# Optimization experiments

Measured on AMD Instinct MI355X. Metric: run time of the kernel, lower is better.

## Reference

```python
import jax, jax.numpy as jnp
import numpy as np

B, T, C = 2, 1024, 2048
N, K = 8, 32            # channels, latents per channel
N_HEAD, N_KV, D = 16, 4, 128  # head_dim = C // n_head; n_rep = 4
N_REP = N_HEAD // N_KV
N_LAYERS = 32


def setup_inputs() -> dict:
    key = jax.random.key(0)
    ks = jax.random.split(key, 8)
    std = 0.02
    proj_std = 0.02 / np.sqrt(2 * N_LAYERS)
    return {
        "x": jax.random.normal(ks[0], (B, T, C), jnp.float32),
        "channel_states": jax.random.normal(ks[1], (B, N, K, C), jnp.float32),
        "channel_mask": jax.random.randint(ks[2], (B, T), 0, N, jnp.int32),
        "Wq": jax.random.normal(ks[3], (C, N_HEAD * D), jnp.float32) * std,
        "Wk": jax.random.normal(ks[4], (C, N_KV * D), jnp.float32) * std,
        "Wv": jax.random.normal(ks[5], (C, N_KV * D), jnp.float32) * std,
        "Wo": jax.random.normal(ks[6], (N_HEAD * D, C), jnp.float32) * proj_std,
        "gate": jax.random.normal(ks[7], (1,), jnp.float32) * 0.02,
    }


def reference(x, channel_states, channel_mask, Wq, Wk, Wv, Wo, gate):
    # x: (B,T,C); channel_states: (B,N,K,C); channel_mask: (B,T) in [0,N)
    b, t, c = x.shape
    # Q projection, grouped for GQA: (B,T,n_kv,n_rep,D)
    q = (x @ Wq).reshape(b, t, N_KV, N_REP, D)
    # Project channel latents ONCE per channel (linear, identical math to the
    # module's redundant per-token re-projection): (B,N,K,n_kv,D)
    k = jnp.einsum("bnkc,ce->bnke", channel_states, Wk).reshape(b, N, K, N_KV, D)
    v = jnp.einsum("bnkc,ce->bnke", channel_states, Wv).reshape(b, N, K, N_KV, D)
    # Per-token channel gather: (B,T,K,n_kv,D)
    batch_idx = jnp.arange(b)[:, None]
    sel_k = k[batch_idx, channel_mask]
    sel_v = v[batch_idx, channel_mask]
    # Tiny-K attention per token; GQA expressed via grouped einsum (no repeat).
    scale = 1.0 / jnp.sqrt(jnp.asarray(D, x.dtype))
    scores = jnp.einsum("btgrd,btkgd->btgrk", q, sel_k) * scale  # (B,T,g,r,K)
    attn = jax.nn.softmax(scores, axis=-1)
    y = jnp.einsum("btgrk,btkgd->btgrd", attn, sel_v).reshape(b, t, c)
    out = (y @ Wo) * jnp.tanh(gate)
    return out


if __name__ == "__main__":
    inp = setup_inputs()
    print(reference(**inp).shape)
```

## Files before the change

kernel.cpp:

```cpp
#include <hip/hip_runtime.h>
#include <hip/hip_bf16.h>

#define BB 2
#define TT 1024
#define CC 2048
#define NCH 8
#define KLAT 32
#define NKV 4
#define NREP 4
#define DD 128
#define MROWS (BB*TT)
#define CSROWS (BB*NCH*KLAT)
#define NBUCKET 16
#define TTILE 8
#define MAXTILES (MROWS/TTILE + NBUCKET)

typedef unsigned short u16;
typedef __attribute__((ext_vector_type(8))) short bf16x8;
typedef __attribute__((ext_vector_type(4))) float f32x4;
typedef __attribute__((ext_vector_type(8))) u16 u16x8;

__device__ __forceinline__ u16 f2bf(float f) {
    unsigned int u = __builtin_bit_cast(unsigned int, f);
    u = (u + 0x7FFFu + ((u >> 16) & 1u)) >> 16;
    return (u16)u;
}

__device__ __forceinline__ void glds16(const u16* g, u16* l) {
    __builtin_amdgcn_global_load_lds(
        (const __attribute__((address_space(1))) void*)g,
        (__attribute__((address_space(3))) void*)l, 16, 0, 0);
}

#define PB_SORT 0
#define PB_X    1
#define PB_CS   (PB_X + 2048)
#define PB_WQ   (PB_CS + 512)
#define PB_WK   (PB_WQ + 1024)
#define PB_WV   (PB_WK + 256)
#define PB_WO   (PB_WV + 256)
#define PB_END  (PB_WO + 1024)

__device__ __forceinline__ void cvt_body(const float* __restrict__ in, u16* __restrict__ out,
                                         int blk, int tid) {
    int i = (blk * 256 + tid) * 8;
    float4 a = *(const float4*)(in + i);
    float4 b = *(const float4*)(in + i + 4);
    u16x8 o;
    o[0]=f2bf(a.x); o[1]=f2bf(a.y); o[2]=f2bf(a.z); o[3]=f2bf(a.w);
    o[4]=f2bf(b.x); o[5]=f2bf(b.y); o[6]=f2bf(b.z); o[7]=f2bf(b.w);
    *(u16x8*)(out + i) = o;
}

__device__ __forceinline__ void tcvt_body(const float* __restrict__ in, u16* __restrict__ out,
                                          int R, int C, int bx, int by, int tid,
                                          u16 (*tile)[65]) {
    const int c0 = bx * 64, r0 = by * 64;
    const int tx = tid & 15, ty = tid >> 4;
#pragma unroll
    for (int p = 0; p < 4; ++p) {
        int r = p * 16 + ty;
        float4 v = *(const float4*)(in + (size_t)(r0 + r) * C + c0 + tx * 4);
        tile[tx*4+0][r] = f2bf(v.x);
        tile[tx*4+1][r] = f2bf(v.y);
        tile[tx*4+2][r] = f2bf(v.z);
        tile[tx*4+3][r] = f2bf(v.w);
    }
    __syncthreads();
    const int oc = tid >> 2, op = tid & 3;
    u16* dst = out + (size_t)(c0 + oc) * R + r0 + op * 16;
    u16x8 v0, v1;
#pragma unroll
    for (int j = 0; j < 8; ++j) { v0[j] = tile[oc][op*16 + j]; v1[j] = tile[oc][op*16 + 8 + j]; }
    *(u16x8*)dst = v0;
    *(u16x8*)(dst + 8) = v1;
}

__global__ void __launch_bounds__(256)
prep_kernel(const float* __restrict__ x, const float* __restrict__ cs,
            const int* __restrict__ cm,
            const float* __restrict__ Wq, const float* __restrict__ Wk,
            const float* __restrict__ Wv, const float* __restrict__ Wo,
            u16* __restrict__ xb, u16* __restrict__ csb,
            u16* __restrict__ wqt, u16* __restrict__ wkvt, u16* __restrict__ wot,
            int* __restrict__ sorted, int4* __restrict__ tiles, int* __restrict__ ntiles)
{
    __shared__ u16 tile[64][65];
    __shared__ int cnt[NBUCKET], cur[NBUCKET];
    const int bid = blockIdx.x;
    const int tid = threadIdx.x;

    if (bid == PB_SORT) {
        if (tid < NBUCKET) cnt[tid] = 0;
        __syncthreads();
        for (int i = tid; i < MROWS; i += 256) {
            int bkt = ((i >> 10) << 3) | cm[i];
            atomicAdd(&cnt[bkt], 1);
        }
        __syncthreads();
        if (tid == 0) {
            int off = 0, nt = 0;
            for (int b2 = 0; b2 < NBUCKET; ++b2) {
                cur[b2] = off;
                for (int o = 0; o < cnt[b2]; o += TTILE)
                    tiles[nt++] = make_int4(b2, off + o, min(TTILE, cnt[b2] - o), 0);
                off += cnt[b2];
            }
            *ntiles = nt;
        }
        __syncthreads();
        for (int i = tid; i < MROWS; i += 256) {
            int bkt = ((i >> 10) << 3) | cm[i];
            int pos = atomicAdd(&cur[bkt], 1);
            sorted[pos] = i;
        }
    } else if (bid < PB_CS) {
        cvt_body(x, xb, bid - PB_X, tid);
    } else if (bid < PB_WQ) {
        cvt_body(cs, csb, bid - PB_CS, tid);
    } else if (bid < PB_WK) {
        int b2 = bid - PB_WQ;
        tcvt_body(Wq, wqt, CC, CC, b2 & 31, b2 >> 5, tid, tile);
    } else if (bid < PB_WV) {
        int b2 = bid - PB_WK;
        tcvt_body(Wk, wkvt, CC, 512, b2 & 7, b2 >> 3, tid, tile);
    } else if (bid < PB_WO) {
        int b2 = bid - PB_WV;
        tcvt_body(Wv, wkvt + (size_t)512 * CC, CC, 512, b2 & 7, b2 >> 3, tid, tile);
    } else {
        int b2 = bid - PB_WO;
        tcvt_body(Wo, wot, CC, CC, b2 & 31, b2 >> 5, tid, tile);
    }
}

#define GK 2048
__device__ __forceinline__ void gemm_core(const u16* __restrict__ A, const u16* __restrict__ Bt,
                                          u16* lds, f32x4 (*acc)[4])
{
    constexpr int BK = 32, STAGE = 8192;
    const int tid  = threadIdx.x;
    const int wave = tid >> 6;
    const int lane = tid & 63;
    const int wm = (wave & 1) * 64;
    const int wn = (wave >> 1) * 64;
    const int ml = lane & 15;
    const int quad = lane >> 4;

#pragma unroll
    for (int i = 0; i < 4; ++i)
#pragma unroll
        for (int j = 0; j < 4; ++j) acc[i][j] = (f32x4){0.f, 0.f, 0.f, 0.f};

    const u16* aptr = A  + (size_t)(tid >> 2) * GK + (tid & 3) * 8;
    const u16* bptr = Bt + (size_t)(tid >> 2) * GK + (tid & 3) * 8;
    const int aoff = wave * 512;
    const int boff = 128 * BK + wave * 512;

#pragma unroll
    for (int s = 0; s < 3; ++s) {
        u16* base = lds + s * STAGE;
        glds16(aptr + s * BK,                   base + aoff);
        glds16(aptr + (size_t)64 * GK + s * BK, base + aoff + 2048);
        glds16(bptr + s * BK,                   base + boff);
        glds16(bptr + (size_t)64 * GK + s * BK, base + boff + 2048);
    }

    for (int k0 = 0; k0 < GK; k0 += BK) {
        u16* cbase = lds + ((k0 / BK) & 3) * STAGE;
        asm volatile("s_waitcnt vmcnt(8)" ::: "memory");
        asm volatile("s_barrier" ::: "memory");
        {
            const int kn = k0 + 3 * BK;
            u16* nbase = lds + (((k0 / BK) + 3) & 3) * STAGE;
            glds16(aptr + kn,                   nbase + aoff);
            glds16(aptr + (size_t)64 * GK + kn, nbase + aoff + 2048);
            glds16(bptr + kn,                   nbase + boff);
            glds16(bptr + (size_t)64 * GK + kn, nbase + boff + 2048);
        }
        bf16x8 afr[4], bfr[4];
#pragma unroll
        for (int i = 0; i < 4; ++i)
            afr[i] = *(const bf16x8*)&cbase[(wm + i * 16 + ml) * BK + quad * 8];
#pragma unroll
        for (int j = 0; j < 4; ++j)
            bfr[j] = *(const bf16x8*)&cbase[128 * BK + (wn + j * 16 + ml) * BK + quad * 8];
#pragma unroll
        for (int i = 0; i < 4; ++i)
#pragma unroll
            for (int j = 0; j < 4; ++j)
                acc[i][j] = __builtin_amdgcn_mfma_f32_16x16x32_bf16(afr[i], bfr[j], acc[i][j], 0, 0, 0);
    }
    asm volatile("s_waitcnt vmcnt(0)" ::: "memory");
}

__global__ void __launch_bounds__(256)
gemm_qkv_kernel(const u16* __restrict__ xb, const u16* __restrict__ wqt, u16* __restrict__ qb,
                const u16* __restrict__ csb, const u16* __restrict__ wkvt,
                u16* __restrict__ kb, u16* __restrict__ vt)
{
    constexpr int STAGE = 8192;
    __shared__ u16 lds[4 * STAGE];
    const int bid = blockIdx.x;
    const int tid = threadIdx.x;
    const int wave = tid >> 6, lane = tid & 63;
    const int wm = (wave & 1) * 64, wn = (wave >> 1) * 64;
    const int ml = lane & 15, quad = lane >> 4;
    const bool isQ = bid < 256;
    const u16 *A, *Bt;
    int m0, n0;
    if (isQ) { m0 = (bid & 15) * 128; n0 = (bid >> 4) * 128; A = xb + (size_t)m0 * GK; Bt = wqt + (size_t)n0 * GK; }
    else     { int b2 = bid - 256; m0 = (b2 & 3) * 128; n0 = (b2 >> 2) * 128; A = csb + (size_t)m0 * GK; Bt = wkvt + (size_t)n0 * GK; }

    f32x4 acc[4][4];
    gemm_core(A, Bt, lds, acc);

#pragma unroll
    for (int i = 0; i < 4; ++i)
#pragma unroll
        for (int j = 0; j < 4; ++j)
#pragma unroll
            for (int rr = 0; rr < 4; ++rr) {
                int gr = m0 + wm + i * 16 + quad * 4 + rr;
                int gc = n0 + wn + j * 16 + ml;
                float val = acc[i][j][rr];
                if (isQ) {
                    qb[(size_t)gr * 2048 + gc] = f2bf(val);
                } else if (gc < 512) {
                    kb[(size_t)gr * 512 + gc] = f2bf(val);
                } else {
                    int g = (gc - 512) >> 7, d = (gc - 512) & 127;
                    int bn = gr >> 5, lat = gr & 31;
                    vt[(((size_t)bn * 4 + g) << 12) + (d << 5) + lat] = f2bf(val);
                }
            }
}

__global__ void __launch_bounds__(256)
gemm_out_kernel(const u16* __restrict__ yb, const u16* __restrict__ wot,
                float* __restrict__ out, const float* __restrict__ gate)
{
    constexpr int STAGE = 8192;
    __shared__ u16 lds[4 * STAGE];
    const int tid = threadIdx.x;
    const int wave = tid >> 6, lane = tid & 63;
    const int wm = (wave & 1) * 64, wn = (wave >> 1) * 64;
    const int ml = lane & 15, quad = lane >> 4;
    const int m0 = blockIdx.x * 128, n0 = blockIdx.y * 128;

    f32x4 acc[4][4];
    gemm_core(yb + (size_t)m0 * GK, wot + (size_t)n0 * GK, lds, acc);

    const float scl = tanhf(gate[0]);
#pragma unroll
    for (int i = 0; i < 4; ++i)
#pragma unroll
        for (int j = 0; j < 4; ++j)
#pragma unroll
            for (int rr = 0; rr < 4; ++rr) {
                int gr = m0 + wm + i * 16 + quad * 4 + rr;
                int gc = n0 + wn + j * 16 + ml;
                out[(size_t)gr * 2048 + gc] = acc[i][j][rr] * scl;
            }
}

#define KSTR 136
#define VSTR 40
__global__ void __launch_bounds__(64)
attn_mfma_kernel(const u16* __restrict__ qb, const u16* __restrict__ kb,
                 const u16* __restrict__ vt, const int* __restrict__ sorted,
                 const int4* __restrict__ tiles, const int* __restrict__ ntiles,
                 u16* __restrict__ yb)
{
    const int tile = blockIdx.x;
    if (tile >= *ntiles) return;
    const int g = blockIdx.y;
    const int4 td = tiles[tile];
    const int bucket = td.x, start = td.y, cnt = td.z;
    const int lane = threadIdx.x;
    const int ml = lane & 15, quad = lane >> 4;

    __shared__ u16 k_lds[32 * KSTR];
    __shared__ u16 v_lds[128 * VSTR];
    __shared__ u16 p_lds[32 * VSTR];
    __shared__ int tok_s[TTILE];

    if (lane < TTILE) tok_s[lane] = (lane < cnt) ? sorted[start + lane] : -1;

    {
        const u16* ksrc = kb + (size_t)bucket * 32 * 512 + g * 128;
        const u16* vsrc = vt + ((size_t)bucket * 4 + g) * 4096;
#pragma unroll
        for (int rr = 0; rr < 8; ++rr) {
            int f = rr * 64 + lane;
            int krow = f >> 4, kc = (f & 15) * 8;
            *(u16x8*)&k_lds[krow * KSTR + kc] = *(const u16x8*)(ksrc + (size_t)krow * 512 + kc);
            int vd = f >> 2, vc = (f & 3) * 8;
            *(u16x8*)&v_lds[vd * VSTR + vc] = *(const u16x8*)(vsrc + (size_t)f * 8);
        }
    }
    __syncthreads();

    f32x4 sc[2][2];
#pragma unroll
    for (int i = 0; i < 2; ++i)
#pragma unroll
        for (int j = 0; j < 2; ++j) sc[i][j] = (f32x4){0.f, 0.f, 0.f, 0.f};
    const int tokA = tok_s[ml & 7];
    const u16* qrow = qb + (size_t)(tokA >= 0 ? tokA : 0) * 2048 + g * 512 + (ml >> 3) * 128;
#pragma unroll
    for (int s = 0; s < 4; ++s) {
        bf16x8 bfr0 = *(const bf16x8*)&k_lds[ml * KSTR + s * 32 + quad * 8];
        bf16x8 bfr1 = *(const bf16x8*)&k_lds[(16 + ml) * KSTR + s * 32 + quad * 8];
#pragma unroll
        for (int i = 0; i < 2; ++i) {
            bf16x8 afr = *(const bf16x8*)(qrow + i * 256 + s * 32 + quad * 8);
            sc[i][0] = __builtin_amdgcn_mfma_f32_16x16x32_bf16(afr, bfr0, sc[i][0], 0, 0, 0);
            sc[i][1] = __builtin_amdgcn_mfma_f32_16x16x32_bf16(afr, bfr1, sc[i][1], 0, 0, 0);
        }
    }

    const float scale = 0.088388347648318447f;
#pragma unroll
    for (int i = 0; i < 2; ++i)
#pragma unroll
        for (int reg = 0; reg < 4; ++reg) {
            float s0 = sc[i][0][reg] * scale;
            float s1 = sc[i][1][reg] * scale;
            float mx = fmaxf(s0, s1);
            mx = fmaxf(mx, __shfl_xor(mx, 1));
            mx = fmaxf(mx, __shfl_xor(mx, 2));
            mx = fmaxf(mx, __shfl_xor(mx, 4));
            mx = fmaxf(mx, __shfl_xor(mx, 8));
            float e0 = __expf(s0 - mx), e1 = __expf(s1 - mx);
            float sm = e0 + e1;
            sm += __shfl_xor(sm, 1);
            sm += __shfl_xor(sm, 2);
            sm += __shfl_xor(sm, 4);
            sm += __shfl_xor(sm, 8);
            float inv = 1.0f / sm;
            int prow = i * 16 + quad * 4 + reg;
            p_lds[prow * VSTR + ml]      = f2bf(e0 * inv);
            p_lds[prow * VSTR + 16 + ml] = f2bf(e1 * inv);
        }
    __syncthreads();

    bf16x8 pfr[2], vfr[8];
    pfr[0] = *(const bf16x8*)&p_lds[ml * VSTR + quad * 8];
    pfr[1] = *(const bf16x8*)&p_lds[(16 + ml) * VSTR + quad * 8];
#pragma unroll
    for (int j = 0; j < 8; ++j)
        vfr[j] = *(const bf16x8*)&v_lds[(j * 16 + ml) * VSTR + quad * 8];
#pragma unroll
    for (int i = 0; i < 2; ++i)
#pragma unroll
        for (int j = 0; j < 8; ++j) {
            f32x4 o = (f32x4){0.f, 0.f, 0.f, 0.f};
            o = __builtin_amdgcn_mfma_f32_16x16x32_bf16(pfr[i], vfr[j], o, 0, 0, 0);
#pragma unroll
            for (int reg = 0; reg < 4; ++reg) {
                int m = quad * 4 + reg;
                int tok = tok_s[m & 7];
                if (tok >= 0) {
                    int r = i * 2 + (m >> 3);
                    yb[(size_t)tok * 2048 + g * 512 + r * 128 + j * 16 + ml] = f2bf(o[reg]);
                }
            }
        }
}

extern "C" void kernel_launch(void* const* d_in, const int* in_sizes, int n_in,
                              void* d_out, int out_size, void* d_ws, size_t ws_size,
                              hipStream_t stream) {
    const float* x    = (const float*)d_in[0];
    const float* cs   = (const float*)d_in[1];
    const int*   cm   = (const int*)d_in[2];
    const float* Wq   = (const float*)d_in[3];
    const float* Wk   = (const float*)d_in[4];
    const float* Wv   = (const float*)d_in[5];
    const float* Wo   = (const float*)d_in[6];
    const float* gate = (const float*)d_in[7];
    float* out = (float*)d_out;

    char* w = (char*)d_ws;
    u16* xb   = (u16*)w;  w += (size_t)MROWS * CC * 2;
    u16* wqt  = (u16*)w;  w += (size_t)CC * CC * 2;
    u16* wot  = (u16*)w;  w += (size_t)CC * CC * 2;
    u16* qb   = (u16*)w;  w += (size_t)MROWS * CC * 2;
    u16* yb   = (u16*)w;  w += (size_t)MROWS * CC * 2;
    u16* csb  = (u16*)w;  w += (size_t)CSROWS * CC * 2;
    u16* wkvt = (u16*)w;  w += (size_t)1024 * CC * 2;
    u16* kb   = (u16*)w;  w += (size_t)CSROWS * 512 * 2;
    u16* vt   = (u16*)w;  w += (size_t)64 * 128 * 32 * 2;
    int* sorted = (int*)w; w += (size_t)MROWS * 4;
    int4* tiles = (int4*)w; w += (size_t)MAXTILES * 16;
    int* ntiles = (int*)w;  w += 4096;

    prep_kernel<<<PB_END, 256, 0, stream>>>(x, cs, cm, Wq, Wk, Wv, Wo,
                                            xb, csb, wqt, wkvt, wot,
                                            sorted, tiles, ntiles);
    gemm_qkv_kernel<<<288, 256, 0, stream>>>(xb, wqt, qb, csb, wkvt, kb, vt);
    attn_mfma_kernel<<<dim3(MAXTILES, 4), 64, 0, stream>>>(qb, kb, vt, sorted, tiles, ntiles, yb);
    gemm_out_kernel<<<dim3(16, 16), 256, 0, stream>>>(yb, wot, out, gate);
}
```

Measured before the change: 196.3 us.

## Fold split-K KV projection into Q GEMM blocks and swizzle GEMM tile order

The QKV launch goes from 288 blocks to 256. Each block first computes its Q tile, then one eighth of the K dimension for a KV tile, writing fp32 partial sums. A new combine kernel sums the eight partials and writes K and the transposed V in bf16. This is meant to remove the second-wave tail that the 32 full-K KV blocks caused, at the cost of an extra launch and fp32 partial-sum traffic. Both GEMMs also use a swizzled block-to-tile mapping, intended to improve L2 reuse of the operands.

```diff
diff --git a/kernel.cpp b/kernel.cpp
--- a/kernel.cpp
+++ b/kernel.cpp
@@ -135,7 +135,7 @@
 
 #define GK 2048
 __device__ __forceinline__ void gemm_core(const u16* __restrict__ A, const u16* __restrict__ Bt,
-                                          u16* lds, f32x4 (*acc)[4])
+                                          u16* lds, f32x4 (*acc)[4], int kiters)
 {
     constexpr int BK = 32, STAGE = 8192;
     const int tid  = threadIdx.x;
@@ -165,13 +165,13 @@
         glds16(bptr + (size_t)64 * GK + s * BK, base + boff + 2048);
     }
 
-    for (int k0 = 0; k0 < GK; k0 += BK) {
-        u16* cbase = lds + ((k0 / BK) & 3) * STAGE;
+    for (int it = 0; it < kiters; ++it) {
+        u16* cbase = lds + (it & 3) * STAGE;
         asm volatile("s_waitcnt vmcnt(8)" ::: "memory");
         asm volatile("s_barrier" ::: "memory");
         {
-            const int kn = k0 + 3 * BK;
-            u16* nbase = lds + (((k0 / BK) + 3) & 3) * STAGE;
+            const int kn = (it + 3) * BK;
+            u16* nbase = lds + ((it + 3) & 3) * STAGE;
             glds16(aptr + kn,                   nbase + aoff);
             glds16(aptr + (size_t)64 * GK + kn, nbase + aoff + 2048);
             glds16(bptr + kn,                   nbase + boff);
@@ -196,7 +196,7 @@
 __global__ void __launch_bounds__(256)
 gemm_qkv_kernel(const u16* __restrict__ xb, const u16* __restrict__ wqt, u16* __restrict__ qb,
                 const u16* __restrict__ csb, const u16* __restrict__ wkvt,
-                u16* __restrict__ kb, u16* __restrict__ vt)
+                float* __restrict__ kvp)
 {
     constexpr int STAGE = 8192;
     __shared__ u16 lds[4 * STAGE];
@@ -205,14 +205,12 @@
     const int wave = tid >> 6, lane = tid & 63;
     const int wm = (wave & 1) * 64, wn = (wave >> 1) * 64;
     const int ml = lane & 15, quad = lane >> 4;
-    const bool isQ = bid < 256;
-    const u16 *A, *Bt;
-    int m0, n0;
-    if (isQ) { m0 = (bid & 15) * 128; n0 = (bid >> 4) * 128; A = xb + (size_t)m0 * GK; Bt = wqt + (size_t)n0 * GK; }
-    else     { int b2 = bid - 256; m0 = (b2 & 3) * 128; n0 = (b2 >> 2) * 128; A = csb + (size_t)m0 * GK; Bt = wkvt + (size_t)n0 * GK; }
+
+    const int swz = (bid & 7) * 32 + (bid >> 3);
+    const int m0 = (swz & 15) * 128, n0 = (swz >> 4) * 128;
 
     f32x4 acc[4][4];
-    gemm_core(A, Bt, lds, acc);
+    gemm_core(xb + (size_t)m0 * GK, wqt + (size_t)n0 * GK, lds, acc, 64);
 
 #pragma unroll
     for (int i = 0; i < 4; ++i)
@@ -222,17 +220,52 @@
             for (int rr = 0; rr < 4; ++rr) {
                 int gr = m0 + wm + i * 16 + quad * 4 + rr;
                 int gc = n0 + wn + j * 16 + ml;
-                float val = acc[i][j][rr];
-                if (isQ) {
-                    qb[(size_t)gr * 2048 + gc] = f2bf(val);
-                } else if (gc < 512) {
-                    kb[(size_t)gr * 512 + gc] = f2bf(val);
-                } else {
-                    int g = (gc - 512) >> 7, d = (gc - 512) & 127;
-                    int bn = gr >> 5, lat = gr & 31;
-                    vt[(((size_t)bn * 4 + g) << 12) + (d << 5) + lat] = f2bf(val);
-                }
+                qb[(size_t)gr * 2048 + gc] = f2bf(acc[i][j][rr]);
             }
+
+    __syncthreads();
+
+    const int tile = bid >> 3, ks = bid & 7;
+    const int m0k = (tile & 3) * 128, n0k = (tile >> 2) * 128;
+    gemm_core(csb + (size_t)m0k * GK + ks * 256,
+              wkvt + (size_t)n0k * GK + ks * 256, lds, acc, 8);
+
+    float* dst = kvp + (size_t)ks * 512 * 1024;
+#pragma unroll
+    for (int i = 0; i < 4; ++i)
+#pragma unroll
+        for (int j = 0; j < 4; ++j)
+#pragma unroll
+            for (int rr = 0; rr < 4; ++rr) {
+                int gr = m0k + wm + i * 16 + quad * 4 + rr;
+                int gc = n0k + wn + j * 16 + ml;
+                dst[(size_t)gr * 1024 + gc] = acc[i][j][rr];
+            }
+}
+
+__global__ void __launch_bounds__(256)
+kv_combine_kernel(const float* __restrict__ kvp, u16* __restrict__ kb, u16* __restrict__ vt)
+{
+    const int idx = (blockIdx.x * 256 + threadIdx.x) * 4;
+    const int r = idx >> 10, c0 = idx & 1023;
+    float4 s = *(const float4*)(kvp + idx);
+#pragma unroll
+    for (int ks = 1; ks < 8; ++ks) {
+        float4 p = *(const float4*)(kvp + (size_t)ks * 524288 + idx);
+        s.x += p.x; s.y += p.y; s.z += p.z; s.w += p.w;
+    }
+    float v4[4] = {s.x, s.y, s.z, s.w};
+#pragma unroll
+    for (int t = 0; t < 4; ++t) {
+        int c = c0 + t;
+        if (c < 512) {
+            kb[(size_t)r * 512 + c] = f2bf(v4[t]);
+        } else {
+            int g = (c - 512) >> 7, d = (c - 512) & 127;
+            int bn = r >> 5, lat = r & 31;
+            vt[(((size_t)bn * 4 + g) << 12) + (d << 5) + lat] = f2bf(v4[t]);
+        }
+    }
 }
 
 __global__ void __launch_bounds__(256)
@@ -245,10 +278,13 @@
     const int wave = tid >> 6, lane = tid & 63;
     const int wm = (wave & 1) * 64, wn = (wave >> 1) * 64;
     const int ml = lane & 15, quad = lane >> 4;
-    const int m0 = blockIdx.x * 128, n0 = blockIdx.y * 128;
+
+    const int bid = blockIdx.x;
+    const int swz = (bid & 7) * 32 + (bid >> 3);
+    const int m0 = (swz & 15) * 128, n0 = (swz >> 4) * 128;
 
     f32x4 acc[4][4];
-    gemm_core(yb + (size_t)m0 * GK, wot + (size_t)n0 * GK, lds, acc);
+    gemm_core(yb + (size_t)m0 * GK, wot + (size_t)n0 * GK, lds, acc, 64);
 
     const float scl = tanhf(gate[0]);
 #pragma unroll
@@ -386,7 +422,6 @@
     u16* wqt  = (u16*)w;  w += (size_t)CC * CC * 2;
     u16* wot  = (u16*)w;  w += (size_t)CC * CC * 2;
     u16* qb   = (u16*)w;  w += (size_t)MROWS * CC * 2;
-    u16* yb   = (u16*)w;  w += (size_t)MROWS * CC * 2;
     u16* csb  = (u16*)w;  w += (size_t)CSROWS * CC * 2;
     u16* wkvt = (u16*)w;  w += (size_t)1024 * CC * 2;
     u16* kb   = (u16*)w;  w += (size_t)CSROWS * 512 * 2;
@@ -394,11 +429,14 @@
     int* sorted = (int*)w; w += (size_t)MROWS * 4;
     int4* tiles = (int4*)w; w += (size_t)MAXTILES * 16;
     int* ntiles = (int*)w;  w += 4096;
+    float* kvp = (float*)w;
+    u16* yb = (u16*)w;      w += (size_t)8 * 512 * 1024 * 4;
 
     prep_kernel<<<PB_END, 256, 0, stream>>>(x, cs, cm, Wq, Wk, Wv, Wo,
                                             xb, csb, wqt, wkvt, wot,
                                             sorted, tiles, ntiles);
-    gemm_qkv_kernel<<<288, 256, 0, stream>>>(xb, wqt, qb, csb, wkvt, kb, vt);
+    gemm_qkv_kernel<<<256, 256, 0, stream>>>(xb, wqt, qb, csb, wkvt, kvp);
+    kv_combine_kernel<<<512, 256, 0, stream>>>(kvp, kb, vt);
     attn_mfma_kernel<<<dim3(MAXTILES, 4), 64, 0, stream>>>(qb, kb, vt, sorted, tiles, ntiles, yb);
-    gemm_out_kernel<<<dim3(16, 16), 256, 0, stream>>>(yb, wot, out, gate);
-}
+    gemm_out_kernel<<<256, 256, 0, stream>>>(yb, wot, out, gate);
+}
```

Measured after the change: 189.4 us. 3.5% less time.
